# Performance work log

Measured on AMD Instinct MI355X. Metric: run time of the kernel, lower is better.

## Reference

```python
import jax, jax.numpy as jnp
import numpy as np

N, F, NEWF = 8192, 128, 64
NEG_INF = -1e10
LEAKY_ALPHA = 0.2


def setup_inputs() -> dict:
    key = jax.random.key(0)
    k1, k2, k3, k4, k5 = jax.random.split(key, 5)
    X = jax.random.normal(k1, (N, F), dtype=jnp.float32)
    A = jax.random.randint(k2, (N, N), 0, 2, dtype=jnp.int32)
    W = jax.random.normal(k3, (F, NEWF), dtype=jnp.float32) * (1.0 / np.sqrt(F))
    a_self = jax.random.normal(k4, (NEWF, 1), dtype=jnp.float32) * (1.0 / np.sqrt(NEWF))
    a_neigh = jax.random.normal(k5, (NEWF, 1), dtype=jnp.float32) * (1.0 / np.sqrt(NEWF))
    return {"X": X, "A": A, "W": W, "a_self": a_self, "a_neigh": a_neigh}


def reference(X, A, W, a_self, a_neigh):
    # Linear transform: [N, newF]
    h = X @ W
    # Additive attention logits: self_attn[i] + neigh_attn[j] -> [N, N]
    self_attn = h @ a_self      # [N, 1]
    neigh_attn = h @ a_neigh    # [N, 1]
    dense = self_attn + neigh_attn.T               # [N, N]
    dense = jax.nn.leaky_relu(dense, LEAKY_ALPHA)
    # Mask: -1e10 where A == 0, else 0
    masked = jnp.where(A == 0, dense + NEG_INF, dense)
    attn = jax.nn.softmax(masked, axis=-1)
    # Dropout is identity at inference (Keras Dropout without training=True)
    out = attn @ h                                  # [N, newF]
    return jax.nn.relu(out)
```

## Files before the change

kernel.cpp:

```cpp
#include <hip/hip_runtime.h>

#define N 8192
#define F 128
#define NEWF 64
#define ALPHA 0.2f
#define JSPLIT 8
#define JW (N / JSPLIT)
#define NCH (JW / 32)
#define RB 64

typedef float f32x4 __attribute__((ext_vector_type(4)));
typedef short short8 __attribute__((ext_vector_type(8)));

__global__ void __launch_bounds__(256) k_pack(const int* __restrict__ A,
                                              unsigned* __restrict__ mask) {
    const int t = threadIdx.x;
    const int row = blockIdx.x * 8 + (t >> 5);
    const int u = t & 31;
    const int js = u >> 2, lg = u & 3;
    const int4* src = (const int4*)(A + (size_t)row * N + js * JW + lg * 8);
    unsigned* dst = mask + (((size_t)row * JSPLIT + js) * 4 + lg) * 8;
#pragma unroll 4
    for (int c4 = 0; c4 < 8; ++c4) {
        unsigned word = 0;
#pragma unroll
        for (int k = 0; k < 4; ++k) {
            const int4* p = src + (size_t)(c4 * 4 + k) * 8;
            int4 a0 = p[0], a1 = p[1];
            unsigned b = 0;
            b |= (a0.x != 0) ? 1u   : 0u;
            b |= (a0.y != 0) ? 2u   : 0u;
            b |= (a0.z != 0) ? 4u   : 0u;
            b |= (a0.w != 0) ? 8u   : 0u;
            b |= (a1.x != 0) ? 16u  : 0u;
            b |= (a1.y != 0) ? 32u  : 0u;
            b |= (a1.z != 0) ? 64u  : 0u;
            b |= (a1.w != 0) ? 128u : 0u;
            word |= b << (8 * k);
        }
        dst[c4] = word;
    }
}

__global__ void k_hsn(const float* __restrict__ X, const float* __restrict__ W,
                      const float* __restrict__ a_self, const float* __restrict__ a_neigh,
                      float* __restrict__ h, float* __restrict__ s, float* __restrict__ n) {
    int row = blockIdx.x * 4 + (threadIdx.x >> 6);
    int l = threadIdx.x & 63;
    const float* xr = X + (size_t)row * F;
    float acc = 0.0f;
#pragma unroll 8
    for (int f = 0; f < F; ++f) acc += xr[f] * W[f * NEWF + l];
    h[(size_t)row * NEWF + l] = acc;
    float ts = acc * a_self[l];
    float tn = acc * a_neigh[l];
#pragma unroll
    for (int off = 32; off; off >>= 1) {
        ts += __shfl_xor(ts, off);
        tn += __shfl_xor(tn, off);
    }
    if (l == 0) { s[row] = ts; n[row] = tn; }
}

__global__ void k_tr(const float* __restrict__ h, unsigned short* __restrict__ hThi,
                     unsigned short* __restrict__ hTlo) {
    __shared__ float tile[64][65];
    const int t = threadIdx.x;
    const int j0 = blockIdx.x * 64;
    {
        const int jr = t >> 2, cs = (t & 3) * 16;
        const float4* src = (const float4*)(h + (size_t)(j0 + jr) * NEWF + cs);
#pragma unroll
        for (int q = 0; q < 4; ++q) {
            float4 v = src[q];
            tile[jr][cs + q * 4 + 0] = v.x; tile[jr][cs + q * 4 + 1] = v.y;
            tile[jr][cs + q * 4 + 2] = v.z; tile[jr][cs + q * 4 + 3] = v.w;
        }
    }
    __syncthreads();
    {
        const int c = t >> 2, js = (t & 3) * 16;
        short8 hi0 = {}, hi1 = {}, lo0 = {}, lo1 = {};
#pragma unroll
        for (int k = 0; k < 16; ++k) {
            float v = tile[js + k][c];
            unsigned xb = __float_as_uint(v);
            short hb = (short)(xb >> 16);
            float lof = v - __uint_as_float(xb & 0xffff0000u);
            short lb = (short)(__float_as_uint(lof) >> 16);
            if (k < 8) { hi0[k] = hb; lo0[k] = lb; }
            else       { hi1[k - 8] = hb; lo1[k - 8] = lb; }
        }
        size_t off = (size_t)c * N + j0 + js;
        *(short8*)(hThi + off)     = hi0;
        *(short8*)(hThi + off + 8) = hi1;
        *(short8*)(hTlo + off)     = lo0;
        *(short8*)(hTlo + off + 8) = lo1;
    }
}

__global__ void k_nmax(const float* __restrict__ n, float* __restrict__ nmax) {
    __shared__ float red[1024];
    int t = threadIdx.x;
    float4 v0 = ((const float4*)n)[t];
    float4 v1 = ((const float4*)n)[t + 1024];
    float m = fmaxf(fmaxf(fmaxf(v0.x, v0.y), fmaxf(v0.z, v0.w)),
                    fmaxf(fmaxf(v1.x, v1.y), fmaxf(v1.z, v1.w)));
    red[t] = m;
    __syncthreads();
    for (int off = 512; off; off >>= 1) {
        if (t < off) red[t] = fmaxf(red[t], red[t + off]);
        __syncthreads();
    }
    if (t == 0) nmax[0] = red[0];
}

__global__ void __launch_bounds__(256, 4) k_main(
        const unsigned* __restrict__ mask, const float* __restrict__ s,
        const float* __restrict__ n, const float* __restrict__ nmaxp,
        const unsigned short* __restrict__ hThi, const unsigned short* __restrict__ hTlo,
        float* __restrict__ pacc, float* __restrict__ pz) {
    __shared__ __align__(16) unsigned short bt[2][2][64][32];

    const int tid = threadIdx.x;
    const int w = tid >> 6, l = tid & 63;
    const int lr = l & 15, lg = l >> 4;

    const int rb = blockIdx.x / JSPLIT;
    const int js = blockIdx.x % JSPLIT;
    const int r0 = rb * RB + w * 16;
    const int jb = js * JW;

    const float sval = s[r0 + lr];
    const float tM = sval + nmaxp[0];
    const float Mv = fmaxf(tM, ALPHA * tM);
    float zacc = 0.0f;

    f32x4 acc0 = {0.f,0.f,0.f,0.f}, acc1 = {0.f,0.f,0.f,0.f};
    f32x4 acc2 = {0.f,0.f,0.f,0.f}, acc3 = {0.f,0.f,0.f,0.f};

    const int srow = tid >> 2, sj = (tid & 3) * 8;
    const short8* ghi = (const short8*)(hThi + (size_t)srow * N + jb + sj);
    const short8* glo = (const short8*)(hTlo + (size_t)srow * N + jb + sj);

    const unsigned* mp = mask + (((size_t)(r0 + lr) * JSPLIT + js) * 4 + lg) * 8;
    unsigned mpref = mp[0];

    {
        short8 vhi = ghi[0];
        short8 vlo = glo[0];
        *(short8*)&bt[0][0][srow][sj] = vhi;
        *(short8*)&bt[0][1][srow][sj] = vlo;
    }
    asm volatile("s_waitcnt lgkmcnt(0)" ::: "memory");
    __builtin_amdgcn_s_barrier();

    const float4* npv = (const float4*)(n + jb + lg * 8);
    float4 nv0 = npv[0], nv1 = npv[1];
    unsigned mword = 0;

    for (int c = 0; c < NCH; ++c) {
        const int p = c & 1;
        const int cn = (c + 1 < NCH) ? c + 1 : 0;

        if ((c & 3) == 0) {
            mword = mpref;
            mpref = mp[((c >> 2) + 1) & 7];
        }
        const unsigned mbyte = (mword >> ((c & 3) * 8)) & 0xffu;

        short8 nhi = ghi[cn * 4];
        short8 nlo = glo[cn * 4];
        float4 nn0 = npv[cn * 8], nn1 = npv[cn * 8 + 1];
        __builtin_amdgcn_sched_barrier(0);

        float nf[8] = {nv0.x, nv0.y, nv0.z, nv0.w, nv1.x, nv1.y, nv1.z, nv1.w};
        short8 ahi, alo;
#pragma unroll
        for (int j = 0; j < 8; ++j) {
            float t  = sval + nf[j];
            float lv = fmaxf(t, ALPHA * t);
            float ex = __expf(lv - Mv);
            ex = (mbyte & (1u << j)) ? ex : 0.0f;
            zacc += ex;
            unsigned xb = __float_as_uint(ex);
            ahi[j] = (short)(xb >> 16);
            float lof = ex - __uint_as_float(xb & 0xffff0000u);
            alo[j] = (short)(__float_as_uint(lof) >> 16);
        }

        short8 B0h = *(const short8*)&bt[p][0][lr +  0][lg * 8];
        short8 B1h = *(const short8*)&bt[p][0][lr + 16][lg * 8];
        short8 B2h = *(const short8*)&bt[p][0][lr + 32][lg * 8];
        short8 B3h = *(const short8*)&bt[p][0][lr + 48][lg * 8];
        short8 B0l = *(const short8*)&bt[p][1][lr +  0][lg * 8];
        short8 B1l = *(const short8*)&bt[p][1][lr + 16][lg * 8];
        short8 B2l = *(const short8*)&bt[p][1][lr + 32][lg * 8];
        short8 B3l = *(const short8*)&bt[p][1][lr + 48][lg * 8];

        acc0 = __builtin_amdgcn_mfma_f32_16x16x32_bf16(ahi, B0h, acc0, 0, 0, 0);
        acc1 = __builtin_amdgcn_mfma_f32_16x16x32_bf16(ahi, B1h, acc1, 0, 0, 0);
        acc2 = __builtin_amdgcn_mfma_f32_16x16x32_bf16(ahi, B2h, acc2, 0, 0, 0);
        acc3 = __builtin_amdgcn_mfma_f32_16x16x32_bf16(ahi, B3h, acc3, 0, 0, 0);
        acc0 = __builtin_amdgcn_mfma_f32_16x16x32_bf16(ahi, B0l, acc0, 0, 0, 0);
        acc1 = __builtin_amdgcn_mfma_f32_16x16x32_bf16(ahi, B1l, acc1, 0, 0, 0);
        acc2 = __builtin_amdgcn_mfma_f32_16x16x32_bf16(ahi, B2l, acc2, 0, 0, 0);
        acc3 = __builtin_amdgcn_mfma_f32_16x16x32_bf16(ahi, B3l, acc3, 0, 0, 0);
        acc0 = __builtin_amdgcn_mfma_f32_16x16x32_bf16(alo, B0h, acc0, 0, 0, 0);
        acc1 = __builtin_amdgcn_mfma_f32_16x16x32_bf16(alo, B1h, acc1, 0, 0, 0);
        acc2 = __builtin_amdgcn_mfma_f32_16x16x32_bf16(alo, B2h, acc2, 0, 0, 0);
        acc3 = __builtin_amdgcn_mfma_f32_16x16x32_bf16(alo, B3h, acc3, 0, 0, 0);

        *(short8*)&bt[p ^ 1][0][srow][sj] = nhi;
        *(short8*)&bt[p ^ 1][1][srow][sj] = nlo;
        asm volatile("s_waitcnt lgkmcnt(0)" ::: "memory");
        __builtin_amdgcn_s_barrier();
        __builtin_amdgcn_sched_barrier(0);

        nv0 = nn0; nv1 = nn1;
    }

    zacc += __shfl_xor(zacc, 16);
    zacc += __shfl_xor(zacc, 32);

    float* pa = pacc + ((size_t)js * N + r0) * NEWF;
#pragma unroll
    for (int r = 0; r < 4; ++r) {
        int row = lg * 4 + r;
        pa[(size_t)row * NEWF +  0 + lr] = acc0[r];
        pa[(size_t)row * NEWF + 16 + lr] = acc1[r];
        pa[(size_t)row * NEWF + 32 + lr] = acc2[r];
        pa[(size_t)row * NEWF + 48 + lr] = acc3[r];
    }
    if (l < 16) pz[(size_t)js * N + r0 + lr] = zacc;
}

__global__ void k_fin(const float* __restrict__ pacc, const float* __restrict__ pz,
                      float* __restrict__ out) {
    int t = blockIdx.x * 256 + threadIdx.x;
    int i = t >> 6, k = t & 63;
    float v = 0.0f, z = 0.0f;
#pragma unroll
    for (int psl = 0; psl < JSPLIT; ++psl) {
        v += pacc[((size_t)psl * N + i) * NEWF + k];
        z += pz[(size_t)psl * N + i];
    }
    out[t] = fmaxf(v / z, 0.0f);
}

extern "C" void kernel_launch(void* const* d_in, const int* in_sizes, int n_in,
                              void* d_out, int out_size, void* d_ws, size_t ws_size,
                              hipStream_t stream) {
    const float* X       = (const float*)d_in[0];
    const int*   A       = (const int*)d_in[1];
    const float* W       = (const float*)d_in[2];
    const float* a_self  = (const float*)d_in[3];
    const float* a_neigh = (const float*)d_in[4];
    float* out = (float*)d_out;

    float* wsf = (float*)d_ws;
    float* h    = wsf;
    float* s    = h + (size_t)N * NEWF;
    float* nv   = s + N;
    float* nmax = nv + N;
    unsigned short* hThi = (unsigned short*)(nmax + 4);
    unsigned short* hTlo = hThi + (size_t)N * NEWF;
    float* pacc = (float*)(hTlo + (size_t)N * NEWF);
    float* pz   = pacc + (size_t)JSPLIT * N * NEWF;
    unsigned* mask = (unsigned*)(pz + (size_t)JSPLIT * N);

    k_pack<<<N / 8,        256, 0, stream>>>(A, mask);
    k_hsn <<<N / 4,        256, 0, stream>>>(X, W, a_self, a_neigh, h, s, nv);
    k_tr  <<<N / 64,       256, 0, stream>>>(h, hThi, hTlo);
    k_nmax<<<1,           1024, 0, stream>>>(nv, nmax);
    k_main<<<(N / RB) * JSPLIT, 256, 0, stream>>>(mask, s, nv, nmax, hThi, hTlo, pacc, pz);
    k_fin <<<(N * NEWF) / 256, 256, 0, stream>>>(pacc, pz, out);
}
```

Baseline: 449.6 us.

## Load B fragments directly from global memory into registers, dropping LDS staging

Each wave now loads its MFMA B-operand fragments (hi/lo bf16 split of h^T) straight from global memory into registers, with register double-buffering of the next chunk. The shared-memory tile, the LDS writes/reads and the per-chunk workgroup barrier are removed. The four waves of a block now each fetch the same B data redundantly, quadrupling global/L2 load traffic, and register pressure rises with 16 short8 live values, which may limit occupancy at launch bounds (256,4).

```diff
diff --git a/kernel.cpp b/kernel.cpp
--- a/kernel.cpp
+++ b/kernel.cpp
@@ -120,8 +120,6 @@
         const float* __restrict__ n, const float* __restrict__ nmaxp,
         const unsigned short* __restrict__ hThi, const unsigned short* __restrict__ hTlo,
         float* __restrict__ pacc, float* __restrict__ pz) {
-    __shared__ __align__(16) unsigned short bt[2][2][64][32];
-
     const int tid = threadIdx.x;
     const int w = tid >> 6, l = tid & 63;
     const int lr = l & 15, lg = l >> 4;
@@ -139,28 +137,25 @@
     f32x4 acc0 = {0.f,0.f,0.f,0.f}, acc1 = {0.f,0.f,0.f,0.f};
     f32x4 acc2 = {0.f,0.f,0.f,0.f}, acc3 = {0.f,0.f,0.f,0.f};
 
-    const int srow = tid >> 2, sj = (tid & 3) * 8;
-    const short8* ghi = (const short8*)(hThi + (size_t)srow * N + jb + sj);
-    const short8* glo = (const short8*)(hTlo + (size_t)srow * N + jb + sj);
+    const short8* gB0h = (const short8*)(hThi + (size_t)(lr +  0) * N + jb + lg * 8);
+    const short8* gB1h = (const short8*)(hThi + (size_t)(lr + 16) * N + jb + lg * 8);
+    const short8* gB2h = (const short8*)(hThi + (size_t)(lr + 32) * N + jb + lg * 8);
+    const short8* gB3h = (const short8*)(hThi + (size_t)(lr + 48) * N + jb + lg * 8);
+    const short8* gB0l = (const short8*)(hTlo + (size_t)(lr +  0) * N + jb + lg * 8);
+    const short8* gB1l = (const short8*)(hTlo + (size_t)(lr + 16) * N + jb + lg * 8);
+    const short8* gB2l = (const short8*)(hTlo + (size_t)(lr + 32) * N + jb + lg * 8);
+    const short8* gB3l = (const short8*)(hTlo + (size_t)(lr + 48) * N + jb + lg * 8);
+    const float4* npv = (const float4*)(n + jb + lg * 8);
 
     const unsigned* mp = mask + (((size_t)(r0 + lr) * JSPLIT + js) * 4 + lg) * 8;
     unsigned mpref = mp[0];
 
-    {
-        short8 vhi = ghi[0];
-        short8 vlo = glo[0];
-        *(short8*)&bt[0][0][srow][sj] = vhi;
-        *(short8*)&bt[0][1][srow][sj] = vlo;
-    }
-    asm volatile("s_waitcnt lgkmcnt(0)" ::: "memory");
-    __builtin_amdgcn_s_barrier();
-
-    const float4* npv = (const float4*)(n + jb + lg * 8);
+    short8 B0h = gB0h[0], B1h = gB1h[0], B2h = gB2h[0], B3h = gB3h[0];
+    short8 B0l = gB0l[0], B1l = gB1l[0], B2l = gB2l[0], B3l = gB3l[0];
     float4 nv0 = npv[0], nv1 = npv[1];
     unsigned mword = 0;
 
     for (int c = 0; c < NCH; ++c) {
-        const int p = c & 1;
         const int cn = (c + 1 < NCH) ? c + 1 : 0;
 
         if ((c & 3) == 0) {
@@ -169,8 +164,10 @@
         }
         const unsigned mbyte = (mword >> ((c & 3) * 8)) & 0xffu;
 
-        short8 nhi = ghi[cn * 4];
-        short8 nlo = glo[cn * 4];
+        short8 nB0h = gB0h[cn * 4], nB1h = gB1h[cn * 4];
+        short8 nB2h = gB2h[cn * 4], nB3h = gB3h[cn * 4];
+        short8 nB0l = gB0l[cn * 4], nB1l = gB1l[cn * 4];
+        short8 nB2l = gB2l[cn * 4], nB3l = gB3l[cn * 4];
         float4 nn0 = npv[cn * 8], nn1 = npv[cn * 8 + 1];
         __builtin_amdgcn_sched_barrier(0);
 
@@ -188,15 +185,6 @@
             float lof = ex - __uint_as_float(xb & 0xffff0000u);
             alo[j] = (short)(__float_as_uint(lof) >> 16);
         }
-
-        short8 B0h = *(const short8*)&bt[p][0][lr +  0][lg * 8];
-        short8 B1h = *(const short8*)&bt[p][0][lr + 16][lg * 8];
-        short8 B2h = *(const short8*)&bt[p][0][lr + 32][lg * 8];
-        short8 B3h = *(const short8*)&bt[p][0][lr + 48][lg * 8];
-        short8 B0l = *(const short8*)&bt[p][1][lr +  0][lg * 8];
-        short8 B1l = *(const short8*)&bt[p][1][lr + 16][lg * 8];
-        short8 B2l = *(const short8*)&bt[p][1][lr + 32][lg * 8];
-        short8 B3l = *(const short8*)&bt[p][1][lr + 48][lg * 8];
 
         acc0 = __builtin_amdgcn_mfma_f32_16x16x32_bf16(ahi, B0h, acc0, 0, 0, 0);
         acc1 = __builtin_amdgcn_mfma_f32_16x16x32_bf16(ahi, B1h, acc1, 0, 0, 0);
@@ -210,14 +198,11 @@
         acc1 = __builtin_amdgcn_mfma_f32_16x16x32_bf16(alo, B1h, acc1, 0, 0, 0);
         acc2 = __builtin_amdgcn_mfma_f32_16x16x32_bf16(alo, B2h, acc2, 0, 0, 0);
         acc3 = __builtin_amdgcn_mfma_f32_16x16x32_bf16(alo, B3h, acc3, 0, 0, 0);
-
-        *(short8*)&bt[p ^ 1][0][srow][sj] = nhi;
-        *(short8*)&bt[p ^ 1][1][srow][sj] = nlo;
-        asm volatile("s_waitcnt lgkmcnt(0)" ::: "memory");
-        __builtin_amdgcn_s_barrier();
         __builtin_amdgcn_sched_barrier(0);
 
-        nv0 = nn0; nv1 = nn1;
+        B0h = nB0h; B1h = nB1h; B2h = nB2h; B3h = nB3h;
+        B0l = nB0l; B1l = nB1l; B2l = nB2l; B3l = nB3l;
+        nv0 = nn0;  nv1 = nn1;
     }
 
     zacc += __shfl_xor(zacc, 16);
```

After: 532.9 us. 18.5% more time.
